# Kernel optimization log

Hardware: AMD Instinct MI355X
Metric: run time of the kernel (lower is better)

## Reference

```python
import jax, jax.numpy as jnp
import numpy as np
import math

D_MODEL = 1024
NUM_HEADS = 16
SEQ = 2048
BATCH = 4


def setup_inputs() -> dict:
    key = jax.random.key(0)
    ks = jax.random.split(key, 7)
    s = 0.02
    return {
        "x": jax.random.normal(ks[0], (BATCH, SEQ, D_MODEL), jnp.float32),
        "Wq": jax.random.normal(ks[1], (D_MODEL, D_MODEL), jnp.float32) * s,
        "bq": jax.random.normal(ks[2], (D_MODEL,), jnp.float32) * s,
        "Wkv": jax.random.normal(ks[3], (D_MODEL, 2 * D_MODEL), jnp.float32) * s,
        "bkv": jax.random.normal(ks[4], (2 * D_MODEL,), jnp.float32) * s,
        "Wo": jax.random.normal(ks[5], (D_MODEL, D_MODEL), jnp.float32) * s,
        "bo": jax.random.normal(ks[6], (D_MODEL,), jnp.float32) * s,
        "decoderMask": 1,
    }


def reference(x, Wq, bq, Wkv, bkv, Wo, bo, decoderMask):
    B, S, D = x.shape
    H = NUM_HEADS
    dh = D // H
    q_ = x @ Wq + bq              # [B,S,D]
    kv_ = x @ Wkv + bkv           # [B,S,2D] (self-attention: m is None)
    # Faithful to source: concat [q_, kv_] then reshape into heads of 3*dh,
    # which interleaves Q/KV projection columns across heads.
    qkv = jnp.concatenate([q_, kv_], axis=-1)          # [B,S,3D]
    qkv = qkv.reshape(B, S, H, 3 * dh).transpose(0, 2, 1, 3)  # [B,H,S,3dh]
    q, k, v = jnp.split(qkv, 3, axis=-1)               # each [B,H,S,dh]
    scaled = jnp.einsum("bhqd,bhkd->bhqk", q, k) / math.sqrt(dh)
    if decoderMask:
        mask = jnp.triu(jnp.full((S, S), -jnp.inf, dtype=scaled.dtype), k=1)
        scaled = scaled + mask
    attn = jax.nn.softmax(scaled, axis=-1)
    vals = jnp.einsum("bhqk,bhkd->bhqd", attn, v)      # [B,H,S,dh]
    vals = vals.transpose(0, 2, 1, 3).reshape(B, S, D)
    return vals @ Wo + bo
```

## Files before the change

kernel.cpp:

```cpp
#include <hip/hip_runtime.h>
#include <cstddef>
#include <cstdint>

#define SEQ   2048
#define BATCH 4
#define DM    1024
#define NH    16
#define DH    64
#define ROWS  (BATCH*SEQ)
#define NC3   3072
#define SM_SCALE 0.18033688f

typedef unsigned short u16;
typedef __attribute__((ext_vector_type(8))) short bf16x8;
typedef __attribute__((ext_vector_type(2))) float f32x2;
typedef __attribute__((ext_vector_type(4))) float f32x4;
typedef __attribute__((ext_vector_type(16))) float f32x16;
typedef __attribute__((ext_vector_type(4))) unsigned u32x4;
typedef __attribute__((ext_vector_type(2))) unsigned u32x2;

union V16 { f32x16 v; f32x2 p[8]; };

__device__ __forceinline__ u16 f2b(float f) {
  union { float f; unsigned u; } v; v.f = f;
  unsigned r = v.u + 0x7fffu + ((v.u >> 16) & 1u);
  return (u16)(r >> 16);
}

__device__ __forceinline__ unsigned cvt_pk_bf16(float lo, float hi) {
  unsigned r;
  asm("v_cvt_pk_bf16_f32 %0, %1, %2" : "=v"(r) : "v"(lo), "v"(hi));
  return r;
}

__device__ __forceinline__ void plswap(unsigned& a, unsigned& b) {
  auto rr = __builtin_amdgcn_permlane32_swap((int)a, (int)b, false, false);
  a = (unsigned)rr[0];
  b = (unsigned)rr[1];
}

__device__ __forceinline__ float ex2(float x) { return __builtin_amdgcn_exp2f(x); }

__device__ __forceinline__ void gld16(const void* g, void* l) {
  __builtin_amdgcn_global_load_lds((const __attribute__((address_space(1))) void*)g,
                                   (__attribute__((address_space(3))) void*)l,
                                   16, 0, 0);
}

__global__ __launch_bounds__(256) void prep_tw_kernel(
    const float* __restrict__ x, const float* __restrict__ bq,
    const float* __restrict__ bkv, u16* __restrict__ xb, float* __restrict__ bc,
    const float* __restrict__ Wq, const float* __restrict__ Wkv,
    const float* __restrict__ Wo, u16* __restrict__ Wt)
{
  __shared__ float t_[32][33];
  const int tid = threadIdx.x;
  if (blockIdx.x < 8192) {
    int i = blockIdx.x * 256 + tid;
    int idx = i * 4;
    float4 v = *(const float4*)(x + idx);
    xb[idx + 0] = f2b(v.x);
    xb[idx + 1] = f2b(v.y);
    xb[idx + 2] = f2b(v.z);
    xb[idx + 3] = f2b(v.w);
    if (i < NC3) bc[i] = (i < DM) ? bq[i] : bkv[i - DM];
  } else {
    const int bid = blockIdx.x - 8192;
    const int n0 = (bid & 127) * 32, k0 = (bid >> 7) * 32;
    const int xcol = tid & 31, yrow = tid >> 5;
    #pragma unroll
    for (int it = 0; it < 4; ++it) {
      int k = k0 + yrow + it * 8;
      int n = n0 + xcol;
      float v;
      if (n < DM)           v = Wq[k * DM + n];
      else if (n < NC3)     v = Wkv[k * (2 * DM) + (n - DM)];
      else                  v = Wo[k * DM + (n - NC3)];
      t_[yrow + it * 8][xcol] = v;
    }
    __syncthreads();
    #pragma unroll
    for (int it = 0; it < 4; ++it) {
      int n = n0 + yrow + it * 8;
      int k = k0 + xcol;
      Wt[(size_t)n * DM + k] = f2b(t_[xcol][yrow + it * 8]);
    }
  }
}

template <int MODE, int N>
__global__ __launch_bounds__(256, 2) void gemm_w128(
    const u16* __restrict__ A, const u16* __restrict__ Bt,
    const float* __restrict__ bias, void* __restrict__ C, u16* __restrict__ Vt)
{
  constexpr int K = 1024;
  constexpr int SLOT = 12288;
  __shared__ alignas(16) u16 lds_[3 * SLOT];

  const int tid = threadIdx.x;
  const int lane = tid & 63, wid = tid >> 6;
  const int wm = wid >> 1, wn = wid & 1;
  const int l15 = lane & 15, lhi = lane >> 4;

  const int bid = blockIdx.x;
  const int xcd = bid & 7, t = bid >> 3;
  const int row0 = (xcd * 4 + (t & 3)) * 256;
  const int col0 = (t >> 2) * 128;

  const int sr = tid >> 2;
  const int scol = (((tid & 3) ^ ((sr >> 1) & 3)) * 8);
  const u16* aSrc = A  + (size_t)(row0 + sr) * K + scol;
  const u16* bSrc = Bt + (size_t)(col0 + sr) * K + scol;
  const int dLin = tid * 8;

  auto stage = [&](int kt, u16* slot) {
    const int ka = kt * 32;
    #pragma unroll
    for (int u = 0; u < 4; ++u)
      gld16(aSrc + (size_t)(u * 64) * K + ka, slot + u * 2048 + dLin);
    #pragma unroll
    for (int u = 0; u < 2; ++u)
      gld16(bSrc + (size_t)(u * 64) * K + ka, slot + 8192 + u * 2048 + dLin);
  };

  const int csw = ((lhi ^ ((l15 >> 1) & 3)) * 8);
  int aoff[8], boff[4];
  #pragma unroll
  for (int m = 0; m < 8; ++m) aoff[m] = (wm * 128 + m * 16 + l15) * 32 + csw;
  #pragma unroll
  for (int n = 0; n < 4; ++n) boff[n] = 8192 + (wn * 64 + n * 16 + l15) * 32 + csw;

  f32x4 acc[8][4];
  #pragma unroll
  for (int m = 0; m < 8; ++m)
    #pragma unroll
    for (int n = 0; n < 4; ++n) { f32x4 z = {0.f, 0.f, 0.f, 0.f}; acc[m][n] = z; }

  u16* const buf0 = lds_;
  u16* const buf1 = lds_ + SLOT;
  u16* const buf2 = lds_ + 2 * SLOT;

  stage(0, buf0); stage(1, buf1);
  asm volatile("s_waitcnt vmcnt(6)" ::: "memory");
  __builtin_amdgcn_s_barrier();

  constexpr int KT = K / 32;
  u16* rb = buf0;
  u16* sb = buf2;
  for (int kt = 0; kt < KT; ++kt) {
    bf16x8 a[8], b[4];
    #pragma unroll
    for (int m = 0; m < 8; ++m) a[m] = *(const bf16x8*)&rb[aoff[m]];
    #pragma unroll
    for (int n = 0; n < 4; ++n) b[n] = *(const bf16x8*)&rb[boff[n]];
    if (kt + 2 < KT) stage(kt + 2, sb);
    __builtin_amdgcn_s_setprio(1);
    #pragma unroll
    for (int m = 0; m < 8; ++m)
      #pragma unroll
      for (int n = 0; n < 4; ++n)
        acc[m][n] = __builtin_amdgcn_mfma_f32_16x16x32_bf16(a[m], b[n], acc[m][n], 0, 0, 0);
    __builtin_amdgcn_s_setprio(0);
    if (kt + 1 < KT) {
      if (kt + 2 < KT) { asm volatile("s_waitcnt vmcnt(6)" ::: "memory"); }
      else             { asm volatile("s_waitcnt vmcnt(0)" ::: "memory"); }
      __builtin_amdgcn_s_barrier();
    }
    rb = (rb == buf2) ? buf0 : rb + SLOT;
    sb = (sb == buf2) ? buf0 : sb + SLOT;
  }

  #pragma unroll
  for (int m = 0; m < 8; ++m) {
    const int row = row0 + wm * 128 + m * 16 + lhi * 4;
    #pragma unroll
    for (int n = 0; n < 4; ++n) {
      const int col = col0 + wn * 64 + n * 16 + l15;
      const float bv = bias[col];
      if (MODE == 0) {
        #pragma unroll
        for (int r = 0; r < 4; ++r)
          ((float*)C)[(size_t)(row + r) * N + col] = acc[m][n][r] + bv;
      } else {
        const int hh = col / 192;
        const int cc = col - hh * 192;
        if (cc < 128) {
          const float qs = (cc < 64) ? SM_SCALE : 1.f;
          #pragma unroll
          for (int r = 0; r < 4; ++r)
            ((u16*)C)[(size_t)(row + r) * N + col] = f2b((acc[m][n][r] + bv) * qs);
        } else {
          u16 wv[4];
          #pragma unroll
          for (int r = 0; r < 4; ++r) wv[r] = f2b(acc[m][n][r] + bv);
          const int bb = row >> 11, jj = row & (SEQ - 1);
          u16* vt = Vt + ((size_t)(bb * NH + hh) * 64 + (cc - 128)) * SEQ + jj;
          u32x2 pv = { (unsigned)wv[0] | ((unsigned)wv[1] << 16),
                       (unsigned)wv[2] | ((unsigned)wv[3] << 16) };
          *(u32x2*)vt = pv;
        }
      }
    }
  }
}

__global__ __launch_bounds__(512, 4) void attn_kernel(
    const u16* __restrict__ qkv, const u16* __restrict__ Vt, u16* __restrict__ ctx)
{
  const int bid = blockIdx.x;
  const int p   = (bid >> 3) & 7;
  const int g   = (bid & 7) + ((bid >> 6) << 3);
  const int h   = g & 15, b = g >> 4;
  const int tid = threadIdx.x;
  const int lane = tid & 63;
  const int hf  = tid >> 8;
  const int wid = (tid >> 6) & 3;
  const int l31 = lane & 31, lhi5 = lane >> 5;

  __shared__ alignas(16) u16 smem_[2 * 16384];
  u16* const smem = smem_ + hf * 16384;

  const int qt  = hf ? (7 - p) : (8 + p);
  const int q0  = qt * 128;
  const int ntL = qt * 2 + 2;
  const int ntMax = (8 + p) * 2 + 2;

  const size_t kv_row = (size_t)(b * NH + h) * 64;
  const int st = tid & 255;
  const int sr = st >> 3, sck = st & 7;
  const int scks = sck ^ (sr & 7);

  const u16* kSrc0 = qkv + (size_t)(b * SEQ + sr) * NC3 + h * 192 + 64 + scks * 8;
  const u16* kSrc1 = kSrc0 + (size_t)32 * NC3;
  const u16* vSrc0 = Vt + (kv_row + sr) * SEQ + scks * 8;
  const u16* vSrc1 = vSrc0 + (size_t)32 * SEQ;
  const int dOff0 = sr * 64 + sck * 8;
  const int dOff1 = (32 + sr) * 64 + sck * 8;

  int koff[4], koff2[4];
  #pragma unroll
  for (int c = 0; c < 4; ++c) {
    koff[c]  = l31 * 64        + (((2 * c + lhi5) ^ (l31 & 7)) * 8);
    koff2[c] = (32 + l31) * 64 + (((2 * c + lhi5) ^ (l31 & 7)) * 8);
  }

  #pragma unroll
  for (int it = 0; it < 4; ++it) {
    int row = it * 32 + sr;
    gld16(qkv + (size_t)(b * SEQ + q0 + row) * NC3 + h * 192 + scks * 8,
          &smem[row * 64 + sck * 8]);
  }
  gld16(kSrc0, &smem[8192 + dOff0]);
  gld16(kSrc1, &smem[8192 + dOff1]);
  gld16(vSrc0, &smem[12288 + dOff0]);
  gld16(vSrc1, &smem[12288 + dOff1]);
  __syncthreads();

  bf16x8 qf[4];
  {
    const int qrow = wid * 32 + l31;
    #pragma unroll
    for (int c = 0; c < 4; ++c)
      qf[c] = *(const bf16x8*)&smem[qrow * 64 + (((2 * c + lhi5) ^ (qrow & 7)) * 8)];
  }
  __syncthreads();

  V16 o0, o1;
  #pragma unroll
  for (int r = 0; r < 16; ++r) { o0.v[r] = 0.f; o1.v[r] = 0.f; }
  float lrow = 0.f;

  const int qw0 = q0 + wid * 32;
  const int qa  = qw0 + l31;
  const int dqb = qa - 4 * lhi5;

  #pragma unroll 1
  for (int jt = 0; jt < ntMax; ++jt) {
    const int j0 = jt * 64;
    const u16* Kb = smem + ((jt & 1) ? 0 : 8192);
    const u16* Vb = smem + ((jt & 1) ? 4096 : 12288);

    if (jt + 1 < ntL) {
      u16* Kn = smem + ((jt & 1) ? 8192 : 0);
      u16* Vn = smem + ((jt & 1) ? 12288 : 4096);
      const size_t kAdv = (size_t)(j0 + 64) * NC3;
      const int    vAdv = j0 + 64;
      gld16(kSrc0 + kAdv, &Kn[dOff0]);
      gld16(kSrc1 + kAdv, &Kn[dOff1]);
      gld16(vSrc0 + vAdv, &Vn[dOff0]);
      gld16(vSrc1 + vAdv, &Vn[dOff1]);
    }

    if (j0 <= qw0 + 31) {
      V16 s0, s1;
      #pragma unroll
      for (int r = 0; r < 16; ++r) { s0.v[r] = 0.f; s1.v[r] = 0.f; }
      __builtin_amdgcn_s_setprio(1);
      #pragma unroll
      for (int c = 0; c < 4; ++c) {
        bf16x8 kf = *(const bf16x8*)&Kb[koff[c]];
        s0.v = __builtin_amdgcn_mfma_f32_32x32x16_bf16(kf, qf[c], s0.v, 0, 0, 0);
      }
      #pragma unroll
      for (int c = 0; c < 4; ++c) {
        bf16x8 kf = *(const bf16x8*)&Kb[koff2[c]];
        s1.v = __builtin_amdgcn_mfma_f32_32x32x16_bf16(kf, qf[c], s1.v, 0, 0, 0);
      }
      __builtin_amdgcn_s_setprio(0);

      if (j0 + 63 > qw0) {
        const int dq = dqb - j0;
        #pragma unroll
        for (int r = 0; r < 16; ++r) {
          const int kvc = (r & 3) + 8 * (r >> 2);
          s0.v[r] = (kvc > dq)      ? -1e30f : s0.v[r];
          s1.v[r] = (kvc + 32 > dq) ? -1e30f : s1.v[r];
        }
      }

      f32x2 sum2 = {0.f, 0.f};
      #pragma unroll
      for (int i = 0; i < 8; ++i) {
        f32x2 e0, e1;
        e0[0] = ex2(s0.p[i][0]); e0[1] = ex2(s0.p[i][1]);
        e1[0] = ex2(s1.p[i][0]); e1[1] = ex2(s1.p[i][1]);
        s0.p[i] = e0; s1.p[i] = e1;
        sum2 += e0 + e1;
      }
      float ps = sum2[0] + sum2[1];
      {
        unsigned a = __builtin_bit_cast(unsigned, ps), bb = a;
        plswap(a, bb);
        ps = __builtin_bit_cast(float, a) + __builtin_bit_cast(float, bb);
      }
      lrow += ps;

      unsigned pk0[8], pk1[8];
      #pragma unroll
      for (int i = 0; i < 4; ++i) {
        pk0[2 * i]     = cvt_pk_bf16(s0.v[4 * i + 0], s0.v[4 * i + 1]);
        pk0[2 * i + 1] = cvt_pk_bf16(s0.v[4 * i + 2], s0.v[4 * i + 3]);
        pk1[2 * i]     = cvt_pk_bf16(s1.v[4 * i + 0], s1.v[4 * i + 1]);
        pk1[2 * i + 1] = cvt_pk_bf16(s1.v[4 * i + 2], s1.v[4 * i + 3]);
      }
      bf16x8 pf[4];
      {
        unsigned a0 = pk0[0], b0 = pk0[2]; plswap(a0, b0);
        unsigned a1 = pk0[1], b1 = pk0[3]; plswap(a1, b1);
        u32x4 w0v = {a0, a1, b0, b1}; pf[0] = __builtin_bit_cast(bf16x8, w0v);
        unsigned a2 = pk0[4], b2 = pk0[6]; plswap(a2, b2);
        unsigned a3 = pk0[5], b3 = pk0[7]; plswap(a3, b3);
        u32x4 w1v = {a2, a3, b2, b3}; pf[1] = __builtin_bit_cast(bf16x8, w1v);
        unsigned a4 = pk1[0], b4 = pk1[2]; plswap(a4, b4);
        unsigned a5 = pk1[1], b5 = pk1[3]; plswap(a5, b5);
        u32x4 w2v = {a4, a5, b4, b5}; pf[2] = __builtin_bit_cast(bf16x8, w2v);
        unsigned a6 = pk1[4], b6 = pk1[6]; plswap(a6, b6);
        unsigned a7 = pk1[5], b7 = pk1[7]; plswap(a7, b7);
        u32x4 w3v = {a6, a7, b6, b7}; pf[3] = __builtin_bit_cast(bf16x8, w3v);
      }

      __builtin_amdgcn_s_setprio(1);
      #pragma unroll
      for (int c = 0; c < 4; ++c) {
        bf16x8 vf = *(const bf16x8*)&Vb[koff[c]];
        o0.v = __builtin_amdgcn_mfma_f32_32x32x16_bf16(vf, pf[c], o0.v, 0, 0, 0);
      }
      #pragma unroll
      for (int c = 0; c < 4; ++c) {
        bf16x8 vf = *(const bf16x8*)&Vb[koff2[c]];
        o1.v = __builtin_amdgcn_mfma_f32_32x32x16_bf16(vf, pf[c], o1.v, 0, 0, 0);
      }
      __builtin_amdgcn_s_setprio(0);
    }
    __syncthreads();
  }

  const float inv = 1.f / lrow;
  u16* crow = ctx + (size_t)(b * SEQ + qa) * DM + h * DH;
  #pragma unroll
  for (int i = 0; i < 4; ++i) {
    u32x2 v0, v1;
    v0[0] = cvt_pk_bf16(o0.v[4 * i + 0] * inv, o0.v[4 * i + 1] * inv);
    v0[1] = cvt_pk_bf16(o0.v[4 * i + 2] * inv, o0.v[4 * i + 3] * inv);
    v1[0] = cvt_pk_bf16(o1.v[4 * i + 0] * inv, o1.v[4 * i + 1] * inv);
    v1[1] = cvt_pk_bf16(o1.v[4 * i + 2] * inv, o1.v[4 * i + 3] * inv);
    *(u32x2*)&crow[8 * i + 4 * lhi5]      = v0;
    *(u32x2*)&crow[32 + 8 * i + 4 * lhi5] = v1;
  }
}

extern "C" void kernel_launch(void* const* d_in, const int* in_sizes, int n_in,
                              void* d_out, int out_size, void* d_ws, size_t ws_size,
                              hipStream_t stream) {
  (void)in_sizes; (void)n_in; (void)out_size; (void)ws_size;
  const float* x   = (const float*)d_in[0];
  const float* Wq  = (const float*)d_in[1];
  const float* bq  = (const float*)d_in[2];
  const float* Wkv = (const float*)d_in[3];
  const float* bkv = (const float*)d_in[4];
  const float* Wo  = (const float*)d_in[5];
  const float* bo  = (const float*)d_in[6];
  float* out = (float*)d_out;

  char* w = (char*)d_ws;
  size_t off = 0;
  auto alloc = [&](size_t bytes) { void* p = w + off; off += (bytes + 255) & ~(size_t)255; return p; };
  u16*   xb   = (u16*)alloc((size_t)ROWS * DM * 2);
  u16*   qkvb = (u16*)alloc((size_t)ROWS * NC3 * 2);
  u16*   Vt   = (u16*)alloc((size_t)BATCH * NH * DH * SEQ * 2);
  u16*   Wt   = (u16*)alloc((size_t)4096 * DM * 2);
  float* bc   = (float*)alloc((size_t)NC3 * 4);
  u16*   ctx  = xb;

  prep_tw_kernel<<<dim3(8192 + 4096), 256, 0, stream>>>(x, bq, bkv, xb, bc, Wq, Wkv, Wo, Wt);
  gemm_w128<1, NC3><<<dim3(768), 256, 0, stream>>>(xb, Wt, bc, qkvb, Vt);
  attn_kernel<<<dim3(512), 512, 0, stream>>>(qkvb, Vt, ctx);
  gemm_w128<0, DM><<<dim3(256), 256, 0, stream>>>(ctx, Wt + (size_t)NC3 * DM, bo, out, nullptr);
}
```

Measured before the change: 158.0 us.

## Fuse fp32-to-bf16 conversion of x into the QKV GEMM A-tile loading

Removes the separate pass that converted x to bf16 in a workspace buffer. The QKV GEMM now loads fp32 x directly into registers, converts it with packed bf16 conversion instructions, and writes it to LDS, with the next tile's global loads issued before the MFMA block. The prep kernel keeps only the weight transpose and bias copy, and ctx gets its own buffer. This saves a full read and write of x, but the GEMM now reads twice the A bytes through registers instead of direct global-to-LDS loads, adding register pressure and extra LDS-write waits each iteration.

After: 163.7 us. +3.6%, slower.

```diff
diff --git a/kernel.cpp b/kernel.cpp
--- a/kernel.cpp
+++ b/kernel.cpp
@@ -47,50 +47,43 @@
                                    16, 0, 0);
 }
 
-__global__ __launch_bounds__(256) void prep_tw_kernel(
-    const float* __restrict__ x, const float* __restrict__ bq,
-    const float* __restrict__ bkv, u16* __restrict__ xb, float* __restrict__ bc,
+__global__ __launch_bounds__(256) void tw_kernel(
     const float* __restrict__ Wq, const float* __restrict__ Wkv,
-    const float* __restrict__ Wo, u16* __restrict__ Wt)
+    const float* __restrict__ Wo, u16* __restrict__ Wt,
+    const float* __restrict__ bq, const float* __restrict__ bkv,
+    float* __restrict__ bc)
 {
   __shared__ float t_[32][33];
   const int tid = threadIdx.x;
-  if (blockIdx.x < 8192) {
-    int i = blockIdx.x * 256 + tid;
-    int idx = i * 4;
-    float4 v = *(const float4*)(x + idx);
-    xb[idx + 0] = f2b(v.x);
-    xb[idx + 1] = f2b(v.y);
-    xb[idx + 2] = f2b(v.z);
-    xb[idx + 3] = f2b(v.w);
-    if (i < NC3) bc[i] = (i < DM) ? bq[i] : bkv[i - DM];
-  } else {
-    const int bid = blockIdx.x - 8192;
-    const int n0 = (bid & 127) * 32, k0 = (bid >> 7) * 32;
-    const int xcol = tid & 31, yrow = tid >> 5;
-    #pragma unroll
-    for (int it = 0; it < 4; ++it) {
-      int k = k0 + yrow + it * 8;
-      int n = n0 + xcol;
-      float v;
-      if (n < DM)           v = Wq[k * DM + n];
-      else if (n < NC3)     v = Wkv[k * (2 * DM) + (n - DM)];
-      else                  v = Wo[k * DM + (n - NC3)];
-      t_[yrow + it * 8][xcol] = v;
-    }
-    __syncthreads();
-    #pragma unroll
-    for (int it = 0; it < 4; ++it) {
-      int n = n0 + yrow + it * 8;
-      int k = k0 + xcol;
-      Wt[(size_t)n * DM + k] = f2b(t_[xcol][yrow + it * 8]);
-    }
+  const int bid = blockIdx.x;
+  if (bid < 12) {
+    int i = bid * 256 + tid;
+    bc[i] = (i < DM) ? bq[i] : bkv[i - DM];
+  }
+  const int n0 = (bid & 127) * 32, k0 = (bid >> 7) * 32;
+  const int xcol = tid & 31, yrow = tid >> 5;
+  #pragma unroll
+  for (int it = 0; it < 4; ++it) {
+    int k = k0 + yrow + it * 8;
+    int n = n0 + xcol;
+    float v;
+    if (n < DM)           v = Wq[k * DM + n];
+    else if (n < NC3)     v = Wkv[k * (2 * DM) + (n - DM)];
+    else                  v = Wo[k * DM + (n - NC3)];
+    t_[yrow + it * 8][xcol] = v;
+  }
+  __syncthreads();
+  #pragma unroll
+  for (int it = 0; it < 4; ++it) {
+    int n = n0 + yrow + it * 8;
+    int k = k0 + xcol;
+    Wt[(size_t)n * DM + k] = f2b(t_[xcol][yrow + it * 8]);
   }
 }
 
 template <int MODE, int N>
 __global__ __launch_bounds__(256, 2) void gemm_w128(
-    const u16* __restrict__ A, const u16* __restrict__ Bt,
+    const void* __restrict__ Asrc, const u16* __restrict__ Bt,
     const float* __restrict__ bias, void* __restrict__ C, u16* __restrict__ Vt)
 {
   constexpr int K = 1024;
@@ -108,20 +101,24 @@
   const int col0 = (t >> 2) * 128;
 
   const int sr = tid >> 2;
-  const int scol = (((tid & 3) ^ ((sr >> 1) & 3)) * 8);
-  const u16* aSrc = A  + (size_t)(row0 + sr) * K + scol;
-  const u16* bSrc = Bt + (size_t)(col0 + sr) * K + scol;
+  const int scolE = (((tid & 3) ^ ((sr >> 1) & 3)) * 8);
+  const u16*   aSrcB = (const u16*)Asrc   + (size_t)(row0 + sr) * K + scolE;
+  const float* aSrcF = (const float*)Asrc + (size_t)(row0 + sr) * K + scolE;
+  const u16*   bSrc  = Bt + (size_t)(col0 + sr) * K + scolE;
   const int dLin = tid * 8;
 
-  auto stage = [&](int kt, u16* slot) {
+  auto stageB = [&](int kt, u16* slot) {
     const int ka = kt * 32;
-    #pragma unroll
-    for (int u = 0; u < 4; ++u)
-      gld16(aSrc + (size_t)(u * 64) * K + ka, slot + u * 2048 + dLin);
     #pragma unroll
     for (int u = 0; u < 2; ++u)
       gld16(bSrc + (size_t)(u * 64) * K + ka, slot + 8192 + u * 2048 + dLin);
   };
+  auto stageAbf = [&](int kt, u16* slot) {
+    const int ka = kt * 32;
+    #pragma unroll
+    for (int u = 0; u < 4; ++u)
+      gld16(aSrcB + (size_t)(u * 64) * K + ka, slot + u * 2048 + dLin);
+  };
 
   const int csw = ((lhi ^ ((l15 >> 1) & 3)) * 8);
   int aoff[8], boff[4];
@@ -140,20 +137,60 @@
   u16* const buf1 = lds_ + SLOT;
   u16* const buf2 = lds_ + 2 * SLOT;
 
-  stage(0, buf0); stage(1, buf1);
-  asm volatile("s_waitcnt vmcnt(6)" ::: "memory");
+  if (MODE == 0) {
+    stageAbf(0, buf0); stageB(0, buf0);
+    stageAbf(1, buf1); stageB(1, buf1);
+    asm volatile("s_waitcnt vmcnt(6)" ::: "memory");
+  } else {
+    float4 p0[8], p1[8];
+    #pragma unroll
+    for (int u = 0; u < 4; ++u) {
+      const float* pA = aSrcF + (size_t)(u * 64) * K;
+      p0[2 * u]     = *(const float4*)pA;
+      p0[2 * u + 1] = *(const float4*)(pA + 4);
+      p1[2 * u]     = *(const float4*)(pA + 32);
+      p1[2 * u + 1] = *(const float4*)(pA + 36);
+    }
+    stageB(0, buf0); stageB(1, buf1);
+    #pragma unroll
+    for (int u = 0; u < 4; ++u) {
+      u32x4 w0, w1;
+      w0[0] = cvt_pk_bf16(p0[2*u].x, p0[2*u].y);   w0[1] = cvt_pk_bf16(p0[2*u].z, p0[2*u].w);
+      w0[2] = cvt_pk_bf16(p0[2*u+1].x, p0[2*u+1].y); w0[3] = cvt_pk_bf16(p0[2*u+1].z, p0[2*u+1].w);
+      w1[0] = cvt_pk_bf16(p1[2*u].x, p1[2*u].y);   w1[1] = cvt_pk_bf16(p1[2*u].z, p1[2*u].w);
+      w1[2] = cvt_pk_bf16(p1[2*u+1].x, p1[2*u+1].y); w1[3] = cvt_pk_bf16(p1[2*u+1].z, p1[2*u+1].w);
+      *(u32x4*)(buf0 + u * 2048 + dLin) = w0;
+      *(u32x4*)(buf1 + u * 2048 + dLin) = w1;
+    }
+    asm volatile("s_waitcnt lgkmcnt(0)" ::: "memory");
+    asm volatile("s_waitcnt vmcnt(2)" ::: "memory");
+  }
   __builtin_amdgcn_s_barrier();
 
   constexpr int KT = K / 32;
   u16* rb = buf0;
   u16* sb = buf2;
   for (int kt = 0; kt < KT; ++kt) {
+    const bool doStage = (kt + 2 < KT);
+    float4 av[8];
+    if (MODE == 1 && doStage) {
+      const int ka = (kt + 2) * 32;
+      #pragma unroll
+      for (int u = 0; u < 4; ++u) {
+        const float* pA = aSrcF + (size_t)(u * 64) * K + ka;
+        av[2 * u]     = *(const float4*)pA;
+        av[2 * u + 1] = *(const float4*)(pA + 4);
+      }
+    }
     bf16x8 a[8], b[4];
     #pragma unroll
     for (int m = 0; m < 8; ++m) a[m] = *(const bf16x8*)&rb[aoff[m]];
     #pragma unroll
     for (int n = 0; n < 4; ++n) b[n] = *(const bf16x8*)&rb[boff[n]];
-    if (kt + 2 < KT) stage(kt + 2, sb);
+    if (doStage) {
+      if (MODE == 0) stageAbf(kt + 2, sb);
+      stageB(kt + 2, sb);
+    }
     __builtin_amdgcn_s_setprio(1);
     #pragma unroll
     for (int m = 0; m < 8; ++m)
@@ -161,9 +198,23 @@
       for (int n = 0; n < 4; ++n)
         acc[m][n] = __builtin_amdgcn_mfma_f32_16x16x32_bf16(a[m], b[n], acc[m][n], 0, 0, 0);
     __builtin_amdgcn_s_setprio(0);
+    if (MODE == 1 && doStage) {
+      #pragma unroll
+      for (int u = 0; u < 4; ++u) {
+        u32x4 w;
+        w[0] = cvt_pk_bf16(av[2*u].x, av[2*u].y);     w[1] = cvt_pk_bf16(av[2*u].z, av[2*u].w);
+        w[2] = cvt_pk_bf16(av[2*u+1].x, av[2*u+1].y); w[3] = cvt_pk_bf16(av[2*u+1].z, av[2*u+1].w);
+        *(u32x4*)(sb + u * 2048 + dLin) = w;
+      }
+    }
     if (kt + 1 < KT) {
-      if (kt + 2 < KT) { asm volatile("s_waitcnt vmcnt(6)" ::: "memory"); }
-      else             { asm volatile("s_waitcnt vmcnt(0)" ::: "memory"); }
+      if (MODE == 1) { asm volatile("s_waitcnt lgkmcnt(0)" ::: "memory"); }
+      if (kt + 2 < KT) {
+        if (MODE == 0) { asm volatile("s_waitcnt vmcnt(6)" ::: "memory"); }
+        else           { asm volatile("s_waitcnt vmcnt(2)" ::: "memory"); }
+      } else {
+        asm volatile("s_waitcnt vmcnt(0)" ::: "memory");
+      }
       __builtin_amdgcn_s_barrier();
     }
     rb = (rb == buf2) ? buf0 : rb + SLOT;
@@ -405,15 +456,14 @@
   char* w = (char*)d_ws;
   size_t off = 0;
   auto alloc = [&](size_t bytes) { void* p = w + off; off += (bytes + 255) & ~(size_t)255; return p; };
-  u16*   xb   = (u16*)alloc((size_t)ROWS * DM * 2);
   u16*   qkvb = (u16*)alloc((size_t)ROWS * NC3 * 2);
   u16*   Vt   = (u16*)alloc((size_t)BATCH * NH * DH * SEQ * 2);
   u16*   Wt   = (u16*)alloc((size_t)4096 * DM * 2);
+  u16*   ctx  = (u16*)alloc((size_t)ROWS * DM * 2);
   float* bc   = (float*)alloc((size_t)NC3 * 4);
-  u16*   ctx  = xb;
-
-  prep_tw_kernel<<<dim3(8192 + 4096), 256, 0, stream>>>(x, bq, bkv, xb, bc, Wq, Wkv, Wo, Wt);
-  gemm_w128<1, NC3><<<dim3(768), 256, 0, stream>>>(xb, Wt, bc, qkvb, Vt);
+
+  tw_kernel<<<dim3(4096), 256, 0, stream>>>(Wq, Wkv, Wo, Wt, bq, bkv, bc);
+  gemm_w128<1, NC3><<<dim3(768), 256, 0, stream>>>(x, Wt, bc, qkvb, Vt);
   attn_kernel<<<dim3(512), 512, 0, stream>>>(qkvb, Vt, ctx);
   gemm_w128<0, DM><<<dim3(256), 256, 0, stream>>>(ctx, Wt + (size_t)NC3 * DM, bo, out, nullptr);
 }
```
